# Kernel optimization log

Hardware: AMD Instinct MI355X
Metric: run time of the kernel (lower is better)

Reference implementation:

```python
import jax, jax.numpy as jnp
import numpy as np
from jax import lax

B, C_IN, T, H, W_SP = 4, 16, 31, 128, 128
HID = 16


def setup_inputs() -> dict:
    key = jax.random.key(0)
    k1, k2 = jax.random.split(key)
    x = jax.random.normal(k1, (B, C_IN, T, H, W_SP), dtype=jnp.float32)
    # Conv3d weight: (out=2*hidden, in, kD, kH, kW), Kaiming-ish scale
    Wt = jax.random.normal(k2, (2 * HID, C_IN, 3, 3, 3), dtype=jnp.float32) * (1.0 / np.sqrt(C_IN * 27))
    b = jnp.zeros((2 * HID,), dtype=jnp.float32)
    return {"x": x, "W": Wt, "b": b}


def reference(x, W, b):
    # 3D conv producing gates: [B, 2*HID, T, H, W]
    gates = lax.conv_general_dilated(
        x, W, window_strides=(1, 1, 1), padding="SAME",
        dimension_numbers=("NCDHW", "OIDHW", "NCDHW"),
    ) + b[None, :, None, None, None]
    Z = jnp.tanh(gates[:, :HID])          # candidate, [B, HID, T, H, W]
    F = jax.nn.sigmoid(gates[:, HID:])    # forget gate

    # fo-pool recurrence over time: h_t = f_t * h_{t-1} + (1 - f_t) * z_t
    Zt = jnp.moveaxis(Z, 2, 0)  # [T, B, HID, H, W]
    Ft = jnp.moveaxis(F, 2, 0)

    def step(h, zf):
        z, f = zf
        h_new = f * h + (1.0 - f) * z
        return h_new, h_new

    h0 = jnp.zeros((B, HID, H, W_SP), dtype=x.dtype)  # state=None -> h starts at 0
    _, hs = lax.scan(step, h0, (Zt, Ft))
    return jnp.moveaxis(hs, 0, 2)  # [B, HID, T, H, W]
```

## Files before the change

kernel.cpp:

```cpp
#include <hip/hip_runtime.h>
#include <hip/hip_bf16.h>
#include <math.h>


namespace {
constexpr int kB = 4, kC = 16, kT = 31, kH = 128, kW = 128, kHid = 16;
constexpr int kHW  = kH * kW;
constexpr int kTHW = kT * kHW;
constexpr int kCell = 8;
constexpr int kOS  = 130 * kCell;
constexpr int kKS  = 2 * kOS;
constexpr int kPS  = 3 * kKS;
constexpr int kSlots = 4;
}

typedef __attribute__((ext_vector_type(8)))  short  short8;
typedef __attribute__((ext_vector_type(4)))  float  floatv4;
typedef __attribute__((ext_vector_type(16))) float  floatx16;

__device__ __forceinline__ unsigned short f2bf(float f) {
    __hip_bfloat16 h = __float2bfloat16(f);
    return __builtin_bit_cast(unsigned short, h);
}

__device__ __forceinline__ int swz(int wp) {
    return (wp & ~7) | ((wp ^ (wp >> 3)) & 7);
}

__global__ __launch_bounds__(256, 2) void qrnn_mfma(
    const float* __restrict__ x, const float* __restrict__ Wt,
    const float* __restrict__ bias, float* __restrict__ out)
{
    __shared__ unsigned short lds[kSlots * kPS];

    const int id  = blockIdx.x;
    const int bh  = (id & 7) * 64 + (id >> 3);
    const int b   = bh >> 7;
    const int h   = bh & (kH - 1);

    const int tid  = threadIdx.x;
    const int lane = tid & 63;
    const int m    = lane & 31;
    const int hi   = lane >> 5;
    const int chi  = hi * 8;
    const int n0   = (tid >> 6) * 32;

    const float* xb = x + b * (kC * kTHW);

    short8 wf[27];
#pragma unroll
    for (int tap = 0; tap < 27; ++tap) {
        short8 v;
#pragma unroll
        for (int j = 0; j < 8; ++j)
            v[j] = (short)f2bf(Wt[m * (kC * 27) + (chi + j) * 27 + tap]);
        wf[tap] = v;
    }

    float st[8], zb[8], fbv[8];
    int ooff[8];
    const int P = n0 + m;
#pragma unroll
    for (int r = 0; r < 8; ++r) {
        const int hid = (r & 3) + 8 * (r >> 2) + 4 * hi;
        zb[r]  = bias[hid];
        fbv[r] = bias[kHid + hid];
        st[r]  = 0.0f;
        ooff[r] = ((b * kHid + hid) * kT) * kHW + h * kW + P;
    }

    const unsigned short* bK0 = lds + hi * kOS + swz(P)     * kCell;
    const unsigned short* bK1 = lds + hi * kOS + swz(P + 1) * kCell;
    const unsigned short* bK2 = lds + hi * kOS + swz(P + 2) * kCell;

    const bool sact = tid < 192;
    const int  skh  = tid >> 6;
    const int  swq  = tid & 31;
    const int  soct = (tid >> 5) & 1;
    const int  shr  = h + skh - 1;
    const bool srow = sact && (shr >= 0) && (shr < kH);
    const float* sbase = xb + (soct * 8) * kTHW + shr * kW + swq * 4;
    unsigned short* cb0 = lds + skh * kKS + soct * kOS;

    int cwoff[4];
#pragma unroll
    for (int q = 0; q < 4; ++q) cwoff[q] = swz(swq * 4 + q + 1) * kCell;

    floatv4 sv[8];

    auto sissue = [&](int tp) {
#pragma unroll
        for (int j = 0; j < 8; ++j) sv[j] = floatv4{0.f, 0.f, 0.f, 0.f};
        if (srow && (unsigned)tp < (unsigned)kT) {
            const float* s = sbase + tp * kHW;
#pragma unroll
            for (int j = 0; j < 8; ++j)
                sv[j] = *(const floatv4*)(s + j * kTHW);
        }
    };
    auto scommit = [&](int tp) {
        if (sact) {
            unsigned short* pl = cb0 + ((tp + 2 * kSlots) & (kSlots - 1)) * kPS;
#pragma unroll
            for (int q = 0; q < 4; ++q) {
                short8 v;
#pragma unroll
                for (int j = 0; j < 8; ++j) v[j] = (short)f2bf(sv[j][q]);
                *(short8*)(pl + cwoff[q]) = v;
            }
        }
    };

    if (tid < 48) {
        const int s = tid / 12, rem = tid % 12;
        const int khh = rem >> 2, q2 = rem & 3;
        const int oct = q2 >> 1;
        const int wp  = (q2 & 1) * 129;
        const short8 z = {0, 0, 0, 0, 0, 0, 0, 0};
        *(short8*)(lds + s * kPS + khh * kKS + oct * kOS + swz(wp) * kCell) = z;
    }

    sissue(-1); scommit(-1);
    sissue(0);  scommit(0);
    sissue(1);

    for (int t = 0; t < kT; ++t) {
        scommit(t + 1);
        __syncthreads();
        sissue(t + 2);

        floatx16 acc = {0,0,0,0,0,0,0,0,0,0,0,0,0,0,0,0};
#pragma unroll
        for (int kd = 0; kd < 3; ++kd) {
            const int soff = ((t + kd + 2 * kSlots - 1) & (kSlots - 1)) * kPS;
#pragma unroll
            for (int kh = 0; kh < 3; ++kh) {
                const int o = soff + kh * kKS;
                const short8 b0 = *(const short8*)(bK0 + o);
                const short8 b1 = *(const short8*)(bK1 + o);
                const short8 b2 = *(const short8*)(bK2 + o);
                acc = __builtin_amdgcn_mfma_f32_32x32x16_bf16(wf[kd*9 + kh*3 + 0], b0, acc, 0, 0, 0);
                acc = __builtin_amdgcn_mfma_f32_32x32x16_bf16(wf[kd*9 + kh*3 + 1], b1, acc, 0, 0, 0);
                acc = __builtin_amdgcn_mfma_f32_32x32x16_bf16(wf[kd*9 + kh*3 + 2], b2, acc, 0, 0, 0);
            }
        }

#pragma unroll
        for (int r = 0; r < 8; ++r) {
            const float zp = acc[r]     + zb[r];
            const float fp = acc[r + 8] + fbv[r];
            const float e2 = __expf(2.0f * zp);
            const float z  = 1.0f - 2.0f * __builtin_amdgcn_rcpf(e2 + 1.0f);
            const float f  = __builtin_amdgcn_rcpf(1.0f + __expf(-fp));
            st[r] = z + f * (st[r] - z);
            out[ooff[r] + t * kHW] = st[r];
        }
    }
}

extern "C" void kernel_launch(void* const* d_in, const int* in_sizes, int n_in,
                              void* d_out, int out_size, void* d_ws, size_t ws_size,
                              hipStream_t stream) {
    const float* x    = (const float*)d_in[0];
    const float* Wt   = (const float*)d_in[1];
    const float* bias = (const float*)d_in[2];
    float* out = (float*)d_out;

    qrnn_mfma<<<dim3(kB * kH), dim3(256), 0, stream>>>(x, Wt, bias, out);
}
```

Baseline: 257.9 us.

## Split each row across single-wave blocks and drop block-level barriers

Each block now runs one wavefront that handles a 32-column tile of an (b,h) row. The grid grows fourfold, and each block stages its own haloed 40-wide input strip into a smaller LDS buffer. Because the block is a single wave, the per-timestep __syncthreads is removed. The cost is that the halo columns are loaded redundantly and the weight fragments are re-converted in every block. The smaller LDS footprint should let more blocks fit per CU, and there is more parallelism overall.

After: 288.3 us. +11.8%, slower.

```diff
diff --git a/kernel.cpp b/kernel.cpp
--- a/kernel.cpp
+++ b/kernel.cpp
@@ -8,7 +8,8 @@
 constexpr int kHW  = kH * kW;
 constexpr int kTHW = kT * kHW;
 constexpr int kCell = 8;
-constexpr int kOS  = 130 * kCell;
+constexpr int kWp  = 40;
+constexpr int kOS  = kWp * kCell;
 constexpr int kKS  = 2 * kOS;
 constexpr int kPS  = 3 * kKS;
 constexpr int kSlots = 4;
@@ -27,23 +28,24 @@
     return (wp & ~7) | ((wp ^ (wp >> 3)) & 7);
 }
 
-__global__ __launch_bounds__(256, 2) void qrnn_mfma(
+__global__ __launch_bounds__(64, 2) void qrnn_mfma(
     const float* __restrict__ x, const float* __restrict__ Wt,
     const float* __restrict__ bias, float* __restrict__ out)
 {
     __shared__ unsigned short lds[kSlots * kPS];
 
-    const int id  = blockIdx.x;
-    const int bh  = (id & 7) * 64 + (id >> 3);
-    const int b   = bh >> 7;
-    const int h   = bh & (kH - 1);
+    const int id   = blockIdx.x;
+    const int orig = (id >> 3) + (id & 7) * 256;
+    const int wt   = orig & 3;
+    const int bh   = orig >> 2;
+    const int b    = bh >> 7;
+    const int h    = bh & (kH - 1);
+    const int w0   = wt * 32;
 
-    const int tid  = threadIdx.x;
-    const int lane = tid & 63;
+    const int lane = threadIdx.x;
     const int m    = lane & 31;
     const int hi   = lane >> 5;
     const int chi  = hi * 8;
-    const int n0   = (tid >> 6) * 32;
 
     const float* xb = x + b * (kC * kTHW);
 
@@ -59,39 +61,40 @@
 
     float st[8], zb[8], fbv[8];
     int ooff[8];
-    const int P = n0 + m;
 #pragma unroll
     for (int r = 0; r < 8; ++r) {
         const int hid = (r & 3) + 8 * (r >> 2) + 4 * hi;
         zb[r]  = bias[hid];
         fbv[r] = bias[kHid + hid];
         st[r]  = 0.0f;
-        ooff[r] = ((b * kHid + hid) * kT) * kHW + h * kW + P;
+        ooff[r] = ((b * kHid + hid) * kT) * kHW + h * kW + w0 + m;
     }
 
-    const unsigned short* bK0 = lds + hi * kOS + swz(P)     * kCell;
-    const unsigned short* bK1 = lds + hi * kOS + swz(P + 1) * kCell;
-    const unsigned short* bK2 = lds + hi * kOS + swz(P + 2) * kCell;
+    const unsigned short* bK0 = lds + hi * kOS + swz(m + 3) * kCell;
+    const unsigned short* bK1 = lds + hi * kOS + swz(m + 4) * kCell;
+    const unsigned short* bK2 = lds + hi * kOS + swz(m + 5) * kCell;
 
-    const bool sact = tid < 192;
-    const int  skh  = tid >> 6;
-    const int  swq  = tid & 31;
-    const int  soct = (tid >> 5) & 1;
+    const bool sact = lane < 60;
+    const int  skh  = lane / 20;
+    const int  srem = lane % 20;
+    const int  sq   = srem >> 1;
+    const int  soct = srem & 1;
+    const int  wq0  = w0 - 4 + sq * 4;
     const int  shr  = h + skh - 1;
-    const bool srow = sact && (shr >= 0) && (shr < kH);
-    const float* sbase = xb + (soct * 8) * kTHW + shr * kW + swq * 4;
+    const bool svalid = sact && wq0 >= 0 && wq0 < kW && shr >= 0 && shr < kH;
+    const float* sbase = xb + (soct * 8) * kTHW + shr * kW + wq0;
     unsigned short* cb0 = lds + skh * kKS + soct * kOS;
 
     int cwoff[4];
 #pragma unroll
-    for (int q = 0; q < 4; ++q) cwoff[q] = swz(swq * 4 + q + 1) * kCell;
+    for (int i = 0; i < 4; ++i) cwoff[i] = swz(sq * 4 + i) * kCell;
 
     floatv4 sv[8];
 
     auto sissue = [&](int tp) {
 #pragma unroll
         for (int j = 0; j < 8; ++j) sv[j] = floatv4{0.f, 0.f, 0.f, 0.f};
-        if (srow && (unsigned)tp < (unsigned)kT) {
+        if (svalid && (unsigned)tp < (unsigned)kT) {
             const float* s = sbase + tp * kHW;
 #pragma unroll
             for (int j = 0; j < 8; ++j)
@@ -102,23 +105,14 @@
         if (sact) {
             unsigned short* pl = cb0 + ((tp + 2 * kSlots) & (kSlots - 1)) * kPS;
 #pragma unroll
-            for (int q = 0; q < 4; ++q) {
+            for (int i = 0; i < 4; ++i) {
                 short8 v;
 #pragma unroll
-                for (int j = 0; j < 8; ++j) v[j] = (short)f2bf(sv[j][q]);
-                *(short8*)(pl + cwoff[q]) = v;
+                for (int j = 0; j < 8; ++j) v[j] = (short)f2bf(sv[j][i]);
+                *(short8*)(pl + cwoff[i]) = v;
             }
         }
     };
-
-    if (tid < 48) {
-        const int s = tid / 12, rem = tid % 12;
-        const int khh = rem >> 2, q2 = rem & 3;
-        const int oct = q2 >> 1;
-        const int wp  = (q2 & 1) * 129;
-        const short8 z = {0, 0, 0, 0, 0, 0, 0, 0};
-        *(short8*)(lds + s * kPS + khh * kKS + oct * kOS + swz(wp) * kCell) = z;
-    }
 
     sissue(-1); scommit(-1);
     sissue(0);  scommit(0);
@@ -126,7 +120,6 @@
 
     for (int t = 0; t < kT; ++t) {
         scommit(t + 1);
-        __syncthreads();
         sissue(t + 2);
 
         floatx16 acc = {0,0,0,0,0,0,0,0,0,0,0,0,0,0,0,0};
@@ -166,5 +159,5 @@
     const float* bias = (const float*)d_in[2];
     float* out = (float*)d_out;
 
-    qrnn_mfma<<<dim3(kB * kH), dim3(256), 0, stream>>>(x, Wt, bias, out);
+    qrnn_mfma<<<dim3(kB * kH * 4), dim3(64), 0, stream>>>(x, Wt, bias, out);
 }
```
